# Kernel tuning notes

Measured on AMD Instinct MI355X. Metric: run time of the kernel, lower is better.

The kernel has to match this reference:

```python
import jax, jax.numpy as jnp
import numpy as np

N_NODES = 100000
N_EDGES = 1600000
D_IN, D_HID, D_OUT = 128, 128, 64


def _mean_agg(h_src_feat, src, dst, num_nodes):
    # gather source features along edges, scatter-sum into destinations,
    # divide by in-degree (clamped to 1, matching DGL zero-degree handling)
    summed = jax.ops.segment_sum(h_src_feat[src], dst, num_segments=num_nodes)
    deg = jax.ops.segment_sum(jnp.ones((src.shape[0],), h_src_feat.dtype), dst,
                              num_segments=num_nodes)
    return summed / jnp.maximum(deg, 1.0)[:, None]


def setup_inputs() -> dict:
    key = jax.random.key(0)
    ks = jax.random.split(key, 8)
    x = jax.random.normal(ks[0], (N_NODES, D_IN), dtype=jnp.float32)
    src = jax.random.randint(ks[1], (N_EDGES,), 0, N_NODES, dtype=jnp.int64)
    dst = jax.random.randint(ks[2], (N_EDGES,), 0, N_NODES, dtype=jnp.int64)
    s1 = 1.0 / np.sqrt(D_IN)
    s2 = 1.0 / np.sqrt(D_HID)
    W_self1 = jax.random.normal(ks[3], (D_IN, D_HID), dtype=jnp.float32) * s1
    W_neigh1 = jax.random.normal(ks[4], (D_IN, D_HID), dtype=jnp.float32) * s1
    b1 = jnp.zeros((D_HID,), dtype=jnp.float32)
    W_self2 = jax.random.normal(ks[5], (D_HID, D_OUT), dtype=jnp.float32) * s2
    W_neigh2 = jax.random.normal(ks[6], (D_HID, D_OUT), dtype=jnp.float32) * s2
    b2 = jnp.zeros((D_OUT,), dtype=jnp.float32)
    return {"x": x, "src": src, "dst": dst,
            "W_self1": W_self1, "W_neigh1": W_neigh1, "b1": b1,
            "W_self2": W_self2, "W_neigh2": W_neigh2, "b2": b2}


def reference(x, src, dst, W_self1, W_neigh1, b1, W_self2, W_neigh2, b2):
    n = x.shape[0]
    # layer 1: SAGEConv(mean) + ReLU (dropout is identity in eval mode)
    agg1 = _mean_agg(x, src, dst, n)
    h = x @ W_self1 + agg1 @ W_neigh1 + b1
    h = jax.nn.relu(h)
    # layer 2: SAGEConv(mean)
    agg2 = _mean_agg(h, src, dst, n)
    out = h @ W_self2 + agg2 @ W_neigh2 + b2
    return out
```

## Files before the change

### kernel.cpp

```cpp
#include <hip/hip_runtime.h>

#define N_NODES 100000
#define N_EDGES 1600000
#define D 128
#define D_OUT 64
#define MAXDEG 64

#define NBUCK 782
#define BSHIFT 7
#define BCAP  3072
#define NBLK_SPLIT 500
#define CHUNK 3200
#define NBLK_CSR NBUCK
#define NBLK_CVT 6250
#define NBLK_PACK 24

typedef __attribute__((ext_vector_type(8))) short short8;
typedef __attribute__((ext_vector_type(4))) float floatx4;
typedef __attribute__((ext_vector_type(2))) float floatx2;

__device__ inline unsigned short f2bf(float f) {
    unsigned u = __builtin_bit_cast(unsigned, f);
    u = (u + 0x7fffu + ((u >> 16) & 1u)) >> 16;
    return (unsigned short)u;
}
__device__ inline float bf2f(unsigned short u) {
    return __builtin_bit_cast(float, (unsigned)u << 16);
}

__device__ inline void pack_ncat(const float* __restrict__ Wa, const float* __restrict__ Wb,
                                 int ncA, int ncB, unsigned short* __restrict__ out, int t) {
    int nnt = (ncA + ncB) >> 4;
    int lane = t & 63;
    int nt = (t >> 6) % nnt;
    int kt = t / (64 * nnt);
    int col = nt * 16 + (lane & 15);
    int k0 = kt * 32 + ((lane >> 4) << 3);
    const float* W = (col < ncA) ? Wa : Wb;
    int nc = (col < ncA) ? ncA : ncB;
    int c  = (col < ncA) ? col : col - ncA;
    unsigned short* dstp = out + (size_t)((kt * nnt + nt) * 64 + lane) * 8;
    #pragma unroll
    for (int j = 0; j < 8; ++j)
        dstp[j] = f2bf(W[(size_t)(k0 + j) * nc + c]);
}

__global__ __launch_bounds__(256) void split_k(
        const int* __restrict__ src, const int* __restrict__ dst,
        int* __restrict__ gcur, int* __restrict__ bucketbuf) {
    __shared__ int cnt[NBUCK];
    __shared__ int base_s[NBUCK];
    __shared__ int dstc[CHUNK];
    const int tid = threadIdx.x;
    const int e0 = blockIdx.x * CHUNK;
    for (int i = tid; i < NBUCK; i += 256) cnt[i] = 0;
    __syncthreads();
    for (int i = tid; i < CHUNK; i += 256) {
        int d = __builtin_nontemporal_load(dst + e0 + i);
        dstc[i] = d;
        atomicAdd(&cnt[d >> BSHIFT], 1);
    }
    __syncthreads();
    for (int i = tid; i < NBUCK; i += 256) {
        int c = cnt[i];
        base_s[i] = c ? atomicAdd(&gcur[i], c) : 0;
        cnt[i] = 0;
    }
    __syncthreads();
    for (int i = tid; i < CHUNK; i += 256) {
        int d = dstc[i];
        int s = __builtin_nontemporal_load(src + e0 + i);
        int bk = d >> BSHIFT;
        int p = base_s[bk] + atomicAdd(&cnt[bk], 1);
        if (p < BCAP)
            bucketbuf[bk * BCAP + p] = ((d & 127) << 17) | s;
    }
}

__global__ __launch_bounds__(256) void prep2(
        const float* __restrict__ x,
        const int* __restrict__ gcur, const int* __restrict__ bucketbuf,
        const float* __restrict__ Ws1, const float* __restrict__ Wn1,
        const float* __restrict__ Ws2, const float* __restrict__ Wn2,
        unsigned short* __restrict__ xb,
        int* __restrict__ dcount, int* __restrict__ csrp,
        unsigned short* __restrict__ Wp1, unsigned short* __restrict__ Wp2) {
    const int tid = threadIdx.x, b = blockIdx.x;
    if (b < NBLK_CSR) {
        __shared__ int lcnt[128];
        if (tid < 128) lcnt[tid] = 0;
        __syncthreads();
        int m = gcur[b]; if (m > BCAP) m = BCAP;
        const int* __restrict__ buf = bucketbuf + b * BCAP;
        for (int i = tid; i < m; i += 256) {
            int v = buf[i];
            int dloc = (v >> 17) & 127, s = v & 0x1FFFF;
            int node = (b << BSHIFT) + dloc;
            int slot = atomicAdd(&lcnt[dloc], 1);
            if (slot < MAXDEG && node < N_NODES)
                csrp[((size_t)node << 6) + slot] = s;
        }
        __syncthreads();
        if (tid < 128) {
            int node = (b << BSHIFT) + tid;
            if (node < N_NODES) {
                int c = lcnt[tid]; if (c > MAXDEG) c = MAXDEG;
                dcount[node] = c;
                int cf = (c + 15) & ~15; if (cf > MAXDEG) cf = MAXDEG;
                int* row = csrp + ((size_t)node << 6);
                for (int k = c; k < cf; ++k) row[k] = 0;
            }
        }
    } else if (b < NBLK_CSR + NBLK_CVT) {
        int i = (b - NBLK_CSR) * 256 + tid;
        const float4* p = (const float4*)x + 2 * (size_t)i;
        float4 a = p[0], c = p[1];
        uint4 u;
        u.x = (unsigned)f2bf(a.x) | ((unsigned)f2bf(a.y) << 16);
        u.y = (unsigned)f2bf(a.z) | ((unsigned)f2bf(a.w) << 16);
        u.z = (unsigned)f2bf(c.x) | ((unsigned)f2bf(c.y) << 16);
        u.w = (unsigned)f2bf(c.z) | ((unsigned)f2bf(c.w) << 16);
        ((uint4*)xb)[i] = u;
    } else {
        int sub = b - (NBLK_CSR + NBLK_CVT);
        if (sub < 16) pack_ncat(Ws1, Wn1, D, D, Wp1, sub * 256 + tid);
        else          pack_ncat(Ws2, Wn2, D_OUT, D_OUT, Wp2, (sub - 16) * 256 + tid);
    }
}

template<int NTA, int NTB, bool OUTA_BF16>
__global__ __launch_bounds__(256) void gemm_dual(
        const unsigned short* __restrict__ A, const unsigned short* __restrict__ Wp,
        const float* __restrict__ bias, void* __restrict__ OutA,
        unsigned char* __restrict__ OutB)
{
    const int NT = NTA + NTB;
    const int wave = threadIdx.x >> 6;
    const int lane = threadIdx.x & 63;
    const int q = lane >> 4, m = lane & 15;

    int row = blockIdx.x * 64 + wave * 16 + m;
    int rowc = (row < N_NODES) ? row : (N_NODES - 1);

    floatx4 acc[NT];
    #pragma unroll
    for (int nt = 0; nt < NT; ++nt) acc[nt] = (floatx4){0.f, 0.f, 0.f, 0.f};

    #pragma unroll
    for (int kt = 0; kt < 4; ++kt) {
        short8 af = *(const short8*)(A + (size_t)rowc * D + kt * 32 + q * 8);
        #pragma unroll
        for (int nt = 0; nt < NT; ++nt) {
            short8 bf = *(const short8*)(Wp + (size_t)((kt * NT + nt) * 64 + lane) * 8);
            acc[nt] = __builtin_amdgcn_mfma_f32_16x16x32_bf16(af, bf, acc[nt], 0, 0, 0);
        }
    }

    const int orow_base = blockIdx.x * 64 + wave * 16 + q * 4;
    #pragma unroll
    for (int nt = 0; nt < NT; ++nt) {
        float bv = (nt < NTA) ? bias[nt * 16 + m] : 0.f;
        #pragma unroll
        for (int i = 0; i < 4; ++i) {
            int orow = orow_base + i;
            if (orow < N_NODES) {
                float v = acc[nt][i];
                if (nt < NTA) {
                    v += bv;
                    if (OUTA_BF16)
                        ((unsigned short*)OutA)[(size_t)orow * (NTA * 16) + nt * 16 + m] = f2bf(v);
                    else
                        ((float*)OutA)[(size_t)orow * (NTA * 16) + nt * 16 + m] = v;
                } else {
                    int pk = __builtin_amdgcn_cvt_pk_fp8_f32(v, v, 0, false);
                    OutB[(size_t)orow * (NTB * 16) + (nt - NTA) * 16 + m] =
                        (unsigned char)(pk & 0xff);
                }
            }
        }
    }
}

template<bool L1>
__global__ __launch_bounds__(256) void agg_add(
        const unsigned char* __restrict__ feat, const int* __restrict__ csrp,
        const int* __restrict__ dcount, const void* __restrict__ self,
        void* __restrict__ out)
{
    const int EPG = L1 ? 4 : 8;
    const int LPE = 64 / EPG;
    const int FSH = L1 ? 7 : 6;
    const int NC  = L1 ? 128 : 64;

    int w = (blockIdx.x * 256 + threadIdx.x) >> 6;
    int lane = threadIdx.x & 63;
    if (w >= N_NODES) return;
    int dg = __builtin_amdgcn_readfirstlane(dcount[w]);
    const int g = lane / LPE;
    const int l = lane % LPE;
    int idxv = csrp[((size_t)w << 6) + lane];

    float a0 = 0.f, a1 = 0.f, a2 = 0.f, a3 = 0.f;
    float a4 = 0.f, a5 = 0.f, a6 = 0.f, a7 = 0.f;
    for (int j = 0; j < dg; j += 16) {
        #pragma unroll
        for (int u = 0; u < 16 / EPG; ++u) {
            int e = j + u * EPG + g;
            int s = __shfl(idxv, e);
            uint2 v = *(const uint2*)(feat + ((size_t)s << FSH) + (l << 3));
            bool ok = e < dg;
            unsigned vx = ok ? v.x : 0u;
            unsigned vy = ok ? v.y : 0u;
            floatx2 f0 = __builtin_amdgcn_cvt_pk_f32_fp8(vx, false);
            floatx2 f1 = __builtin_amdgcn_cvt_pk_f32_fp8(vx, true);
            floatx2 f2 = __builtin_amdgcn_cvt_pk_f32_fp8(vy, false);
            floatx2 f3 = __builtin_amdgcn_cvt_pk_f32_fp8(vy, true);
            a0 += f0.x; a1 += f0.y; a2 += f1.x; a3 += f1.y;
            a4 += f2.x; a5 += f2.y; a6 += f3.x; a7 += f3.y;
        }
    }
    #pragma unroll
    for (int step = 0; step < 3; ++step) {
        int delta = 32 >> step;
        if (delta >= LPE) {
            a0 += __shfl_down(a0, delta); a1 += __shfl_down(a1, delta);
            a2 += __shfl_down(a2, delta); a3 += __shfl_down(a3, delta);
            a4 += __shfl_down(a4, delta); a5 += __shfl_down(a5, delta);
            a6 += __shfl_down(a6, delta); a7 += __shfl_down(a7, delta);
        }
    }
    if (g == 0) {
        float invd = (dg > 0) ? 1.0f / (float)dg : 1.0f;
        if (L1) {
            const unsigned short* sp = (const unsigned short*)self + (size_t)w * NC + l * 8;
            short8 sv = *(const short8*)sp;
            short8 hv;
            float acc[8] = {a0,a1,a2,a3,a4,a5,a6,a7};
            #pragma unroll
            for (int c = 0; c < 8; ++c) {
                float hval = bf2f((unsigned short)sv[c]) + acc[c] * invd;
                hval = fmaxf(hval, 0.f);
                hv[c] = (short)f2bf(hval);
            }
            *(short8*)((unsigned short*)out + (size_t)w * NC + l * 8) = hv;
        } else {
            const float* sp = (const float*)self + (size_t)w * NC + l * 8;
            float4 s0 = *(const float4*)sp;
            float4 s1 = *(const float4*)(sp + 4);
            float4 o0, o1;
            o0.x = s0.x + a0 * invd; o0.y = s0.y + a1 * invd;
            o0.z = s0.z + a2 * invd; o0.w = s0.w + a3 * invd;
            o1.x = s1.x + a4 * invd; o1.y = s1.y + a5 * invd;
            o1.z = s1.z + a6 * invd; o1.w = s1.w + a7 * invd;
            float* op = (float*)out + (size_t)w * NC + l * 8;
            *(float4*)op = o0;
            *(float4*)(op + 4) = o1;
        }
    }
}

extern "C" void kernel_launch(void* const* d_in, const int* in_sizes, int n_in,
                              void* d_out, int out_size, void* d_ws, size_t ws_size,
                              hipStream_t stream) {
    const float* x   = (const float*)d_in[0];
    const int*   src = (const int*)d_in[1];
    const int*   dst = (const int*)d_in[2];
    const float* Ws1 = (const float*)d_in[3];
    const float* Wn1 = (const float*)d_in[4];
    const float* b1  = (const float*)d_in[5];
    const float* Ws2 = (const float*)d_in[6];
    const float* Wn2 = (const float*)d_in[7];
    const float* b2  = (const float*)d_in[8];
    float* out = (float*)d_out;

    const size_t nd = (size_t)N_NODES * D;
    unsigned short* xb  = (unsigned short*)d_ws;
    unsigned short* h   = xb;
    unsigned short* xs  = xb + nd;
    float*          tmp = (float*)xs;
    unsigned char*  y8  = (unsigned char*)(xs + nd);
    unsigned char*  z8  = y8;
    int* dcount = (int*)(y8 + nd);
    int* csrp   = dcount + N_NODES;
    int* gcur   = csrp + (size_t)N_NODES * MAXDEG;
    int* bucketbuf = gcur + 1024;
    unsigned short* Wp1 = (unsigned short*)(bucketbuf + (size_t)NBUCK * BCAP);
    unsigned short* Wp2 = Wp1 + 32768;

    hipMemsetAsync(gcur, 0, NBUCK * sizeof(int), stream);

    split_k<<<NBLK_SPLIT, 256, 0, stream>>>(src, dst, gcur, bucketbuf);
    prep2<<<NBLK_CSR + NBLK_CVT + NBLK_PACK, 256, 0, stream>>>(
        x, gcur, bucketbuf, Ws1, Wn1, Ws2, Wn2, xb, dcount, csrp, Wp1, Wp2);

    const int gemm_blocks = (N_NODES + 63) / 64;
    const int agg_blocks  = (N_NODES * 64 + 255) / 256;

    gemm_dual<8, 8, true ><<<gemm_blocks, 256, 0, stream>>>(xb, Wp1, b1, xs, y8);
    agg_add<true ><<<agg_blocks, 256, 0, stream>>>(y8, csrp, dcount, xs, h);
    gemm_dual<4, 4, false><<<gemm_blocks, 256, 0, stream>>>(h, Wp2, b2, tmp, z8);
    agg_add<false><<<agg_blocks, 256, 0, stream>>>(z8, csrp, dcount, tmp, out);
}
```

Before: 320.0 us.

## Fuse x bf16 conversion into GEMM, use zero-row padding, widen aggregation lanes

Removes the separate fp32-to-bf16 conversion pass over x. The first GEMM now reads fp32 x directly and converts in registers, which cuts a full read and write of the feature matrix. Weight packing moves into the edge-split kernel, and CSR building becomes its own kernel. Padded CSR slots now point to a zeroed dummy row, so the aggregation drops the per-edge validity masking. Aggregation lanes now load 4 fp8 bytes each with more lanes per edge and fewer edges in flight per wave, which may lower memory-level parallelism.

```diff
diff --git a/kernel.cpp b/kernel.cpp
--- a/kernel.cpp
+++ b/kernel.cpp
@@ -11,9 +11,7 @@
 #define BCAP  3072
 #define NBLK_SPLIT 500
 #define CHUNK 3200
-#define NBLK_CSR NBUCK
-#define NBLK_CVT 6250
-#define NBLK_PACK 24
+#define NBLK_PACK 25
 
 typedef __attribute__((ext_vector_type(8))) short short8;
 typedef __attribute__((ext_vector_type(4))) float floatx4;
@@ -24,8 +22,8 @@
     u = (u + 0x7fffu + ((u >> 16) & 1u)) >> 16;
     return (unsigned short)u;
 }
-__device__ inline float bf2f(unsigned short u) {
-    return __builtin_bit_cast(float, (unsigned)u << 16);
+__device__ inline float bf2f(unsigned u16) {
+    return __builtin_bit_cast(float, u16 << 16);
 }
 
 __device__ inline void pack_ncat(const float* __restrict__ Wa, const float* __restrict__ Wb,
@@ -45,92 +43,86 @@
         dstp[j] = f2bf(W[(size_t)(k0 + j) * nc + c]);
 }
 
-__global__ __launch_bounds__(256) void split_k(
+__global__ __launch_bounds__(256) void split_pack(
         const int* __restrict__ src, const int* __restrict__ dst,
-        int* __restrict__ gcur, int* __restrict__ bucketbuf) {
+        int* __restrict__ gcur, int* __restrict__ bucketbuf,
+        const float* __restrict__ Ws1, const float* __restrict__ Wn1,
+        const float* __restrict__ Ws2, const float* __restrict__ Wn2,
+        unsigned short* __restrict__ Wp1, unsigned short* __restrict__ Wp2,
+        unsigned char* __restrict__ y8, unsigned char* __restrict__ z8) {
     __shared__ int cnt[NBUCK];
     __shared__ int base_s[NBUCK];
     __shared__ int dstc[CHUNK];
     const int tid = threadIdx.x;
-    const int e0 = blockIdx.x * CHUNK;
-    for (int i = tid; i < NBUCK; i += 256) cnt[i] = 0;
+    const int b = blockIdx.x;
+    if (b < NBLK_SPLIT) {
+        const int e0 = b * CHUNK;
+        for (int i = tid; i < NBUCK; i += 256) cnt[i] = 0;
+        __syncthreads();
+        for (int i = tid; i < CHUNK; i += 256) {
+            int d = __builtin_nontemporal_load(dst + e0 + i);
+            dstc[i] = d;
+            atomicAdd(&cnt[d >> BSHIFT], 1);
+        }
+        __syncthreads();
+        for (int i = tid; i < NBUCK; i += 256) {
+            int c = cnt[i];
+            base_s[i] = c ? atomicAdd(&gcur[i], c) : 0;
+            cnt[i] = 0;
+        }
+        __syncthreads();
+        for (int i = tid; i < CHUNK; i += 256) {
+            int d = dstc[i];
+            int s = __builtin_nontemporal_load(src + e0 + i);
+            int bk = d >> BSHIFT;
+            int p = base_s[bk] + atomicAdd(&cnt[bk], 1);
+            if (p < BCAP)
+                bucketbuf[bk * BCAP + p] = ((d & 127) << 17) | s;
+        }
+    } else {
+        int sub = b - NBLK_SPLIT;
+        if (sub < 16)      pack_ncat(Ws1, Wn1, D, D, Wp1, sub * 256 + tid);
+        else if (sub < 24) pack_ncat(Ws2, Wn2, D_OUT, D_OUT, Wp2, (sub - 16) * 256 + tid);
+        else {
+            if (tid < 32)       ((unsigned*)(y8 + (size_t)N_NODES * 128))[tid] = 0;
+            else if (tid < 48)  ((unsigned*)(z8 + (size_t)N_NODES * 64))[tid - 32] = 0;
+        }
+    }
+}
+
+__global__ __launch_bounds__(256) void csr_build(
+        const int* __restrict__ gcur, const int* __restrict__ bucketbuf,
+        int* __restrict__ dcount, int* __restrict__ csrp) {
+    __shared__ int lcnt[128];
+    const int tid = threadIdx.x, b = blockIdx.x;
+    if (tid < 128) lcnt[tid] = 0;
     __syncthreads();
-    for (int i = tid; i < CHUNK; i += 256) {
-        int d = __builtin_nontemporal_load(dst + e0 + i);
-        dstc[i] = d;
-        atomicAdd(&cnt[d >> BSHIFT], 1);
+    int m = gcur[b]; if (m > BCAP) m = BCAP;
+    const int* __restrict__ buf = bucketbuf + b * BCAP;
+    for (int i = tid; i < m; i += 256) {
+        int v = buf[i];
+        int dloc = (v >> 17) & 127, s = v & 0x1FFFF;
+        int node = (b << BSHIFT) + dloc;
+        int slot = atomicAdd(&lcnt[dloc], 1);
+        if (slot < MAXDEG && node < N_NODES)
+            csrp[((size_t)node << 6) + slot] = s;
     }
     __syncthreads();
-    for (int i = tid; i < NBUCK; i += 256) {
-        int c = cnt[i];
-        base_s[i] = c ? atomicAdd(&gcur[i], c) : 0;
-        cnt[i] = 0;
-    }
-    __syncthreads();
-    for (int i = tid; i < CHUNK; i += 256) {
-        int d = dstc[i];
-        int s = __builtin_nontemporal_load(src + e0 + i);
-        int bk = d >> BSHIFT;
-        int p = base_s[bk] + atomicAdd(&cnt[bk], 1);
-        if (p < BCAP)
-            bucketbuf[bk * BCAP + p] = ((d & 127) << 17) | s;
-    }
-}
-
-__global__ __launch_bounds__(256) void prep2(
-        const float* __restrict__ x,
-        const int* __restrict__ gcur, const int* __restrict__ bucketbuf,
-        const float* __restrict__ Ws1, const float* __restrict__ Wn1,
-        const float* __restrict__ Ws2, const float* __restrict__ Wn2,
-        unsigned short* __restrict__ xb,
-        int* __restrict__ dcount, int* __restrict__ csrp,
-        unsigned short* __restrict__ Wp1, unsigned short* __restrict__ Wp2) {
-    const int tid = threadIdx.x, b = blockIdx.x;
-    if (b < NBLK_CSR) {
-        __shared__ int lcnt[128];
-        if (tid < 128) lcnt[tid] = 0;
-        __syncthreads();
-        int m = gcur[b]; if (m > BCAP) m = BCAP;
-        const int* __restrict__ buf = bucketbuf + b * BCAP;
-        for (int i = tid; i < m; i += 256) {
-            int v = buf[i];
-            int dloc = (v >> 17) & 127, s = v & 0x1FFFF;
-            int node = (b << BSHIFT) + dloc;
-            int slot = atomicAdd(&lcnt[dloc], 1);
-            if (slot < MAXDEG && node < N_NODES)
-                csrp[((size_t)node << 6) + slot] = s;
-        }
-        __syncthreads();
-        if (tid < 128) {
-            int node = (b << BSHIFT) + tid;
-            if (node < N_NODES) {
-                int c = lcnt[tid]; if (c > MAXDEG) c = MAXDEG;
-                dcount[node] = c;
-                int cf = (c + 15) & ~15; if (cf > MAXDEG) cf = MAXDEG;
-                int* row = csrp + ((size_t)node << 6);
-                for (int k = c; k < cf; ++k) row[k] = 0;
-            }
-        }
-    } else if (b < NBLK_CSR + NBLK_CVT) {
-        int i = (b - NBLK_CSR) * 256 + tid;
-        const float4* p = (const float4*)x + 2 * (size_t)i;
-        float4 a = p[0], c = p[1];
-        uint4 u;
-        u.x = (unsigned)f2bf(a.x) | ((unsigned)f2bf(a.y) << 16);
-        u.y = (unsigned)f2bf(a.z) | ((unsigned)f2bf(a.w) << 16);
-        u.z = (unsigned)f2bf(c.x) | ((unsigned)f2bf(c.y) << 16);
-        u.w = (unsigned)f2bf(c.z) | ((unsigned)f2bf(c.w) << 16);
-        ((uint4*)xb)[i] = u;
-    } else {
-        int sub = b - (NBLK_CSR + NBLK_CVT);
-        if (sub < 16) pack_ncat(Ws1, Wn1, D, D, Wp1, sub * 256 + tid);
-        else          pack_ncat(Ws2, Wn2, D_OUT, D_OUT, Wp2, (sub - 16) * 256 + tid);
-    }
-}
-
-template<int NTA, int NTB, bool OUTA_BF16>
+    if (tid < 128) {
+        int node = (b << BSHIFT) + tid;
+        if (node < N_NODES) {
+            int c = lcnt[tid]; if (c > MAXDEG) c = MAXDEG;
+            dcount[node] = c;
+            int cf = (c + 15) & ~15; if (cf > MAXDEG) cf = MAXDEG;
+            int* row = csrp + ((size_t)node << 6);
+            for (int k = c; k < cf; ++k) row[k] = N_NODES;
+        }
+    }
+}
+
+template<int NTA, int NTB, bool AF32, bool OUTA_BF16>
 __global__ __launch_bounds__(256) void gemm_dual(
-        const unsigned short* __restrict__ A, const unsigned short* __restrict__ Wp,
+        const void* __restrict__ A, const unsigned short* __restrict__ Wp,
         const float* __restrict__ bias, void* __restrict__ OutA,
         unsigned char* __restrict__ OutB)
 {
@@ -148,7 +140,19 @@
 
     #pragma unroll
     for (int kt = 0; kt < 4; ++kt) {
-        short8 af = *(const short8*)(A + (size_t)rowc * D + kt * 32 + q * 8);
+        short8 af;
+        if (AF32) {
+            const float* xr = (const float*)A + (size_t)rowc * D + kt * 32 + q * 8;
+            float4 f0 = *(const float4*)xr;
+            float4 f1 = *(const float4*)(xr + 4);
+            af[0] = (short)f2bf(f0.x); af[1] = (short)f2bf(f0.y);
+            af[2] = (short)f2bf(f0.z); af[3] = (short)f2bf(f0.w);
+            af[4] = (short)f2bf(f1.x); af[5] = (short)f2bf(f1.y);
+            af[6] = (short)f2bf(f1.z); af[7] = (short)f2bf(f1.w);
+        } else {
+            af = *(const short8*)((const unsigned short*)A +
+                                  (size_t)rowc * D + kt * 32 + q * 8);
+        }
         #pragma unroll
         for (int nt = 0; nt < NT; ++nt) {
             short8 bf = *(const short8*)(Wp + (size_t)((kt * NT + nt) * 64 + lane) * 8);
@@ -187,8 +191,8 @@
         const int* __restrict__ dcount, const void* __restrict__ self,
         void* __restrict__ out)
 {
-    const int EPG = L1 ? 4 : 8;
-    const int LPE = 64 / EPG;
+    const int LPE = L1 ? 32 : 16;
+    const int EPG = 64 / LPE;
     const int FSH = L1 ? 7 : 6;
     const int NC  = L1 ? 128 : 64;
 
@@ -200,61 +204,43 @@
     const int l = lane % LPE;
     int idxv = csrp[((size_t)w << 6) + lane];
 
-    float a0 = 0.f, a1 = 0.f, a2 = 0.f, a3 = 0.f;
-    float a4 = 0.f, a5 = 0.f, a6 = 0.f, a7 = 0.f;
+    floatx2 ac0 = (floatx2){0.f, 0.f};
+    floatx2 ac1 = (floatx2){0.f, 0.f};
     for (int j = 0; j < dg; j += 16) {
         #pragma unroll
         for (int u = 0; u < 16 / EPG; ++u) {
-            int e = j + u * EPG + g;
-            int s = __shfl(idxv, e);
-            uint2 v = *(const uint2*)(feat + ((size_t)s << FSH) + (l << 3));
-            bool ok = e < dg;
-            unsigned vx = ok ? v.x : 0u;
-            unsigned vy = ok ? v.y : 0u;
-            floatx2 f0 = __builtin_amdgcn_cvt_pk_f32_fp8(vx, false);
-            floatx2 f1 = __builtin_amdgcn_cvt_pk_f32_fp8(vx, true);
-            floatx2 f2 = __builtin_amdgcn_cvt_pk_f32_fp8(vy, false);
-            floatx2 f3 = __builtin_amdgcn_cvt_pk_f32_fp8(vy, true);
-            a0 += f0.x; a1 += f0.y; a2 += f1.x; a3 += f1.y;
-            a4 += f2.x; a5 += f2.y; a6 += f3.x; a7 += f3.y;
-        }
-    }
-    #pragma unroll
-    for (int step = 0; step < 3; ++step) {
-        int delta = 32 >> step;
-        if (delta >= LPE) {
-            a0 += __shfl_down(a0, delta); a1 += __shfl_down(a1, delta);
-            a2 += __shfl_down(a2, delta); a3 += __shfl_down(a3, delta);
-            a4 += __shfl_down(a4, delta); a5 += __shfl_down(a5, delta);
-            a6 += __shfl_down(a6, delta); a7 += __shfl_down(a7, delta);
-        }
+            int s = __shfl(idxv, j + u * EPG + g);
+            unsigned v = *(const unsigned*)(feat + ((size_t)s << FSH) + (l << 2));
+            ac0 += __builtin_amdgcn_cvt_pk_f32_fp8(v, false);
+            ac1 += __builtin_amdgcn_cvt_pk_f32_fp8(v, true);
+        }
+    }
+    #pragma unroll
+    for (int delta = 32; delta >= LPE; delta >>= 1) {
+        ac0.x += __shfl_down(ac0.x, delta); ac0.y += __shfl_down(ac0.y, delta);
+        ac1.x += __shfl_down(ac1.x, delta); ac1.y += __shfl_down(ac1.y, delta);
     }
     if (g == 0) {
         float invd = (dg > 0) ? 1.0f / (float)dg : 1.0f;
         if (L1) {
-            const unsigned short* sp = (const unsigned short*)self + (size_t)w * NC + l * 8;
-            short8 sv = *(const short8*)sp;
-            short8 hv;
-            float acc[8] = {a0,a1,a2,a3,a4,a5,a6,a7};
-            #pragma unroll
-            for (int c = 0; c < 8; ++c) {
-                float hval = bf2f((unsigned short)sv[c]) + acc[c] * invd;
-                hval = fmaxf(hval, 0.f);
-                hv[c] = (short)f2bf(hval);
-            }
-            *(short8*)((unsigned short*)out + (size_t)w * NC + l * 8) = hv;
+            uint2 sv = *(const uint2*)((const unsigned short*)self + (size_t)w * NC + l * 4);
+            float h0 = bf2f(sv.x & 0xffffu)  + ac0.x * invd;
+            float h1 = bf2f(sv.x >> 16)      + ac0.y * invd;
+            float h2 = bf2f(sv.y & 0xffffu)  + ac1.x * invd;
+            float h3 = bf2f(sv.y >> 16)      + ac1.y * invd;
+            h0 = fmaxf(h0, 0.f); h1 = fmaxf(h1, 0.f);
+            h2 = fmaxf(h2, 0.f); h3 = fmaxf(h3, 0.f);
+            uint2 pv;
+            pv.x = (unsigned)f2bf(h0) | ((unsigned)f2bf(h1) << 16);
+            pv.y = (unsigned)f2bf(h2) | ((unsigned)f2bf(h3) << 16);
+            *(uint2*)((unsigned short*)out + (size_t)w * NC + l * 4) = pv;
         } else {
-            const float* sp = (const float*)self + (size_t)w * NC + l * 8;
+            const float* sp = (const float*)self + (size_t)w * NC + l * 4;
             float4 s0 = *(const float4*)sp;
-            float4 s1 = *(const float4*)(sp + 4);
-            float4 o0, o1;
-            o0.x = s0.x + a0 * invd; o0.y = s0.y + a1 * invd;
-            o0.z = s0.z + a2 * invd; o0.w = s0.w + a3 * invd;
-            o1.x = s1.x + a4 * invd; o1.y = s1.y + a5 * invd;
-            o1.z = s1.z + a6 * invd; o1.w = s1.w + a7 * invd;
-            float* op = (float*)out + (size_t)w * NC + l * 8;
-            *(float4*)op = o0;
-            *(float4*)(op + 4) = o1;
+            float4 o;
+            o.x = s0.x + ac0.x * invd; o.y = s0.y + ac0.y * invd;
+            o.z = s0.z + ac1.x * invd; o.w = s0.w + ac1.y * invd;
+            *(float4*)((float*)out + (size_t)w * NC + l * 4) = o;
         }
     }
 }
@@ -274,13 +260,12 @@
     float* out = (float*)d_out;
 
     const size_t nd = (size_t)N_NODES * D;
-    unsigned short* xb  = (unsigned short*)d_ws;
-    unsigned short* h   = xb;
-    unsigned short* xs  = xb + nd;
+    unsigned short* h   = (unsigned short*)d_ws;
+    unsigned short* xs  = h + nd;
     float*          tmp = (float*)xs;
     unsigned char*  y8  = (unsigned char*)(xs + nd);
-    unsigned char*  z8  = y8;
-    int* dcount = (int*)(y8 + nd);
+    unsigned char*  z8  = y8 + (size_t)(N_NODES + 1) * D;
+    int* dcount = (int*)(z8 + (size_t)(N_NODES + 1) * D_OUT);
     int* csrp   = dcount + N_NODES;
     int* gcur   = csrp + (size_t)N_NODES * MAXDEG;
     int* bucketbuf = gcur + 1024;
@@ -289,15 +274,15 @@
 
     hipMemsetAsync(gcur, 0, NBUCK * sizeof(int), stream);
 
-    split_k<<<NBLK_SPLIT, 256, 0, stream>>>(src, dst, gcur, bucketbuf);
-    prep2<<<NBLK_CSR + NBLK_CVT + NBLK_PACK, 256, 0, stream>>>(
-        x, gcur, bucketbuf, Ws1, Wn1, Ws2, Wn2, xb, dcount, csrp, Wp1, Wp2);
+    split_pack<<<NBLK_SPLIT + NBLK_PACK, 256, 0, stream>>>(
+        src, dst, gcur, bucketbuf, Ws1, Wn1, Ws2, Wn2, Wp1, Wp2, y8, z8);
+    csr_build<<<NBUCK, 256, 0, stream>>>(gcur, bucketbuf, dcount, csrp);
 
     const int gemm_blocks = (N_NODES + 63) / 64;
     const int agg_blocks  = (N_NODES * 64 + 255) / 256;
 
-    gemm_dual<8, 8, true ><<<gemm_blocks, 256, 0, stream>>>(xb, Wp1, b1, xs, y8);
+    gemm_dual<8, 8, true,  true ><<<gemm_blocks, 256, 0, stream>>>(x, Wp1, b1, xs, y8);
     agg_add<true ><<<agg_blocks, 256, 0, stream>>>(y8, csrp, dcount, xs, h);
-    gemm_dual<4, 4, false><<<gemm_blocks, 256, 0, stream>>>(h, Wp2, b2, tmp, z8);
+    gemm_dual<4, 4, false, false><<<gemm_blocks, 256, 0, stream>>>(h, Wp2, b2, tmp, z8);
     agg_add<false><<<agg_blocks, 256, 0, stream>>>(z8, csrp, dcount, tmp, out);
 }
```

Measured after the change: 298.9 us. 6.6% less time.
